# Performance work log

Hardware: AMD Instinct MI355X
Metric: run time of the kernel (lower is better)

## Reference

```python
import jax, jax.numpy as jnp
import numpy as np

NPG = 32          # nodes per graph
G = 2048          # number of graphs
V = G * NPG       # 65536 nodes
DEG = 4           # incoming edges per node
E = V * DEG       # 262144 edges
H = 200           # hidden feat size
NODE_IN = 74
EDGE_IN = 12
N_LAYERS = 5
T = 2             # readout GRU timesteps


def setup_inputs() -> dict:
    key = jax.random.key(0)
    ks = jax.random.split(key, 24)

    def p(k, shape, s=0.1):
        return jax.random.normal(k, shape, jnp.float32) * s

    node_feat = jax.random.normal(ks[0], (V, NODE_IN), jnp.float32)
    edge_feat = jax.random.normal(ks[1], (E, EDGE_IN), jnp.float32)
    # graph structure: each node gets DEG incoming edges from random nodes of the same graph
    dst = jnp.repeat(jnp.arange(V, dtype=jnp.int32), DEG)
    src = (dst // NPG) * NPG + jax.random.randint(ks[2], (E,), 0, NPG, dtype=jnp.int32)
    graph_id = jnp.arange(V, dtype=jnp.int32) // NPG

    return dict(
        node_feat=node_feat, edge_feat=edge_feat, src=src, dst=dst, graph_id=graph_id,
        node_W=p(ks[3], (NODE_IN, H)), node_b=p(ks[4], (H,)),
        edge_W=p(ks[5], (EDGE_IN, H)), edge_b=p(ks[6], (H,)),
        gnn_W=p(ks[7], (N_LAYERS, H, H)), gnn_b=p(ks[8], (N_LAYERS, H)),
        lg_W=p(ks[9], (T, 2 * H, 1)), lg_b=p(ks[10], (T, 1)),
        pr_W=p(ks[11], (T, H, H)), pr_b=p(ks[12], (T, H)),
        W_ih=p(ks[13], (T, 3 * H, H)), W_hh=p(ks[14], (T, 3 * H, H)),
        b_ih=p(ks[15], (T, 3 * H)), b_hh=p(ks[16], (T, 3 * H)),
    )


def reference(node_feat, edge_feat, src, dst, graph_id,
              node_W, node_b, edge_W, edge_b, gnn_W, gnn_b,
              lg_W, lg_b, pr_W, pr_b, W_ih, W_hh, b_ih, b_hh):
    # embedding (dropout layers are identity at eval)
    h = node_feat @ node_W + node_b        # [V, H]
    eh = edge_feat @ edge_W + edge_b       # [E, H]

    # GCN layers with edge features, aggr == 'no_relu'
    for i in range(N_LAYERS):
        m = h[src] + eh                                              # u_add_e, [E, H]
        mx = jax.ops.segment_max(m, dst, num_segments=V)             # edge_softmax over incoming edges
        ex = jnp.exp(m - mx[dst])
        den = jax.ops.segment_sum(ex, dst, num_segments=V)
        a = ex / den[dst]
        agg = jax.ops.segment_sum(m * a, dst, num_segments=V)        # [V, H]
        h = jax.nn.relu(agg @ gnn_W[i] + gnn_b[i]) + h               # mlp + relu + residual

    # AttentiveFP readout
    gf = jax.ops.segment_sum(h, graph_id, num_segments=G)            # [G, H]
    for t in range(T):
        zin = jnp.concatenate([jax.nn.relu(gf)[graph_id], h], axis=1)  # [V, 2H]
        z = jax.nn.leaky_relu(zin @ lg_W[t] + lg_b[t])                  # [V, 1]
        zmax = jax.ops.segment_max(z, graph_id, num_segments=G)        # softmax_nodes
        e = jnp.exp(z - zmax[graph_id])
        a = e / jax.ops.segment_sum(e, graph_id, num_segments=G)[graph_id]
        hv = h @ pr_W[t] + pr_b[t]
        ctx = jax.nn.elu(jax.ops.segment_sum(hv * a, graph_id, num_segments=G))  # [G, H]
        # torch GRUCell: gates ordered (r, z, n)
        gi = ctx @ W_ih[t].T + b_ih[t]
        gh = gf @ W_hh[t].T + b_hh[t]
        ir, iz, inn = jnp.split(gi, 3, axis=1)
        hr, hz, hn = jnp.split(gh, 3, axis=1)
        r = jax.nn.sigmoid(ir + hr)
        u = jax.nn.sigmoid(iz + hz)
        n = jnp.tanh(inn + r * hn)
        gf = (1.0 - u) * n + u * gf
    return gf
```

## Files before the change

kernel.cpp:

```cpp
#include <hip/hip_runtime.h>
#include <hip/hip_bf16.h>
#include <math.h>

#define V 65536
#define G 2048
#define NPG 32
#define DEG 4
#define NE (V*DEG)
#define H 200
#define NODE_IN 74
#define EDGE_IN 12
#define NL 5

#define KP 224
#define NP 208
#define AGSC 101
#define EK 32
#define HS 200

typedef __attribute__((ext_vector_type(8))) short short8;
typedef __attribute__((ext_vector_type(4))) float floatx4;
typedef __attribute__((ext_vector_type(2))) float float2v;

__device__ __forceinline__ float sigmoidf_(float x) { return 1.f / (1.f + __expf(-x)); }

__device__ __forceinline__ unsigned f2bf_bits(float f) {
    unsigned u = __float_as_uint(f);
    return (u + 0x7fffu + ((u >> 16) & 1u)) >> 16;
}
__device__ __forceinline__ float bf2f(unsigned bits) { return __uint_as_float(bits << 16); }
__device__ __forceinline__ unsigned lo_bits(float f, unsigned hb) {
    return f2bf_bits(f - bf2f(hb));
}

__global__ __launch_bounds__(256) void k_node_embed(const float* __restrict__ nf,
                                                    const float* __restrict__ W,
                                                    const float* __restrict__ b,
                                                    float* __restrict__ h) {
    __shared__ float fs[16][NODE_IN];
    const int tid = threadIdx.x;
    const int base = blockIdx.x * 16;
    for (int p = tid; p < 16 * NODE_IN; p += 256) {
        int n = p / NODE_IN, i = p - n * NODE_IN;
        fs[n][i] = nf[(base + n) * NODE_IN + i];
    }
    __syncthreads();
    const int j = tid;
    if (j < H) {
        float acc[16];
#pragma unroll
        for (int n = 0; n < 16; n++) acc[n] = 0.f;
        for (int i = 0; i < NODE_IN; i++) {
            float w = W[i * H + j];
#pragma unroll
            for (int n = 0; n < 16; n++) acc[n] = fmaf(fs[n][i], w, acc[n]);
        }
        float bj = b[j];
        for (int n = 0; n < 16; n++) h[(base + n) * H + j] = acc[n] + bj;
    }
}

#define EFB (NE / 256)
#define SEG_W (NL * NP * KP)
#define SEG_EW NP
__global__ __launch_bounds__(256) void k_prep(const float* __restrict__ ef,
                                              const float* __restrict__ gnnW,
                                              const float* __restrict__ eW,
                                              const float* __restrict__ eb,
                                              unsigned short* __restrict__ Aedge,
                                              unsigned short* __restrict__ WtHi,
                                              unsigned short* __restrict__ WtLo,
                                              unsigned short* __restrict__ eWp) {
    __shared__ float efs[256 * EDGE_IN];
    const int tid = threadIdx.x, blk = blockIdx.x;
    if (blk < EFB) {
        const float4* gs = (const float4*)(ef + (size_t)blk * 256 * EDGE_IN);
        float4* ds = (float4*)efs;
        for (int p = tid; p < 256 * EDGE_IN / 4; p += 256) ds[p] = gs[p];
        __syncthreads();
        unsigned hb[EDGE_IN], lb[EDGE_IN];
        for (int k = 0; k < EDGE_IN; k++) {
            float v = efs[tid * EDGE_IN + k];
            hb[k] = f2bf_bits(v);
            lb[k] = lo_bits(v, hb[k]);
        }
        unsigned w[16];
        for (int i = 0; i < 6; i++) w[i] = hb[2 * i] | (hb[2 * i + 1] << 16);
        for (int i = 0; i < 6; i++) w[6 + i] = lb[2 * i] | (lb[2 * i + 1] << 16);
        w[12] = 0x3F803F80u;
        w[13] = 0u; w[14] = 0u; w[15] = 0u;
        uint4* dst = (uint4*)(Aedge + ((size_t)blk * 256 + tid) * EK);
        dst[0] = make_uint4(w[0], w[1], w[2], w[3]);
        dst[1] = make_uint4(w[4], w[5], w[6], w[7]);
        dst[2] = make_uint4(w[8], w[9], w[10], w[11]);
        dst[3] = make_uint4(w[12], w[13], w[14], w[15]);
        return;
    }
    int idx = (blk - EFB) * 256 + tid;
    if (idx < SEG_W) {
        int l = idx / (NP * KP);
        int rem = idx - l * (NP * KP);
        int n = rem / KP;
        int k = rem - n * KP;
        float w = (n < H && k < H) ? gnnW[l * H * H + k * H + n] : 0.f;
        unsigned hb = f2bf_bits(w);
        WtHi[idx] = (unsigned short)hb;
        WtLo[idx] = (unsigned short)lo_bits(w, hb);
        return;
    }
    idx -= SEG_W;
    if (idx < SEG_EW) {
        int t = idx;
        unsigned short row[64];
        for (int i = 0; i < 64; i++) row[i] = 0;
        if (t < H) {
            for (int k = 0; k < EDGE_IN; k++) {
                float w = eW[k * H + t];
                unsigned hb = f2bf_bits(w);
                row[k] = (unsigned short)hb;
                row[12 + k] = (unsigned short)hb;
                row[32 + k] = (unsigned short)lo_bits(w, hb);
            }
            float e = eb[t];
            unsigned ebh = f2bf_bits(e);
            row[24] = (unsigned short)ebh;
            row[25] = (unsigned short)lo_bits(e, ebh);
        }
        for (int i = 0; i < 64; i++) eWp[t * 64 + i] = row[i];
    }
}

__global__ __launch_bounds__(256, 4) void k_mega(float* __restrict__ h,
                                                 const unsigned short* __restrict__ Aedge,
                                                 const unsigned short* __restrict__ eWp,
                                                 const int* __restrict__ src,
                                                 const unsigned short* __restrict__ WtHi,
                                                 const unsigned short* __restrict__ WtLo,
                                                 const float* __restrict__ gnn_b,
                                                 float* __restrict__ gf_out) {
    __shared__ alignas(16) float h_s[NPG * HS];
    __shared__ alignas(16) unsigned int aggc[NPG * AGSC];
    __shared__ alignas(16) unsigned int zpad[8];
    __shared__ unsigned char src_s[NPG * DEG];
    const int g = blockIdx.x, tid = threadIdx.x;
    const int nbase = g * NPG, ebase = g * NPG * DEG;

    const int wave = tid >> 6, lane = tid & 63;
    const int l15 = lane & 15, quad = lane >> 4;
    const int ntcnt = (wave == 0) ? 4 : 3;

    const int mtA = wave * 2, mtB = mtA + 1;
    short8 afA, afB;
    {
        const unsigned short* abase = Aedge + (size_t)ebase * EK;
        afA = *(const short8*)&abase[(16 * mtA + l15) * EK + quad * 8];
        afB = *(const short8*)&abase[(16 * mtB + l15) * EK + quad * 8];
    }
    if (tid < NPG * DEG) src_s[tid] = (unsigned char)(src[ebase + tid] - nbase);
    if (tid < 8) zpad[tid] = 0u;
    {
        const float4* hsrc = (const float4*)(h + (size_t)nbase * H);
        float4* hdst = (float4*)h_s;
        for (int p = tid; p < NPG * H / 4; p += 256) hdst[p] = hsrc[p];
    }
    __syncthreads();

    const int nodeA = 4 * mtA + quad, nodeB = 4 * mtB + quad;
    int gsA[4], gsB[4];
#pragma unroll
    for (int e = 0; e < 4; e++) {
        gsA[e] = (int)src_s[nodeA * 4 + e] * HS;
        gsB[e] = (int)src_s[nodeB * 4 + e] * HS;
    }
    unsigned short* rowA = (unsigned short*)(aggc + nodeA * AGSC);
    unsigned short* rowB = (unsigned short*)(aggc + nodeB * AGSC);
    const float2v L2E2 = {1.4426950408889634f, 1.4426950408889634f};

    const int ntb0[3] = {0, 6, 10};
    const int ntb1[3] = {6, 10, 13};
    const int ksb0[3] = {0, 3, 5};
    const int ksb1[3] = {3, 5, 7};

    for (int l = 0; l < NL; l++) {
        floatx4 acc2[2][4];
#pragma unroll
        for (int mt = 0; mt < 2; mt++)
#pragma unroll
            for (int i = 0; i < 4; i++) acc2[mt][i] = (floatx4){0.f, 0.f, 0.f, 0.f};

        const unsigned short* WH = WtHi + (size_t)l * NP * KP;
        const unsigned short* WL = WtLo + (size_t)l * NP * KP;

        for (int ch = 0; ch < 3; ch++) {
            const int nt0 = ntb0[ch], nt1 = ntb1[ch];
            const int ks0 = ksb0[ch], ks1 = ksb1[ch];

            for (int nt = nt0; nt < nt1; nt++) {
                const int jj = nt * 16 + l15;
                const int jloc = jj - nt0 * 16;
                const int jc = jj < H ? jj : H - 1;
                const int colo = (jloc >> 3) * 16 + (jloc & 7);
                const bool val = (jj < H);
                short8 b1 = *(const short8*)&eWp[(size_t)jj * 64 + quad * 8];
                short8 b2 = *(const short8*)&eWp[(size_t)jj * 64 + 32 + quad * 8];

                auto unit = [&](short8 af, const int* gs, unsigned short* rowp) {
                    floatx4 z = (floatx4){0.f, 0.f, 0.f, 0.f};
                    z = __builtin_amdgcn_mfma_f32_16x16x32_bf16(af, b1, z, 0, 0, 0);
                    z = __builtin_amdgcn_mfma_f32_16x16x32_bf16(af, b2, z, 0, 0, 0);
                    floatx4 mh4;
#pragma unroll
                    for (int e = 0; e < 4; e++) mh4[e] = h_s[gs[e] + jc];
                    float2v mlo = __builtin_shufflevector(z, z, 0, 1) +
                                  __builtin_shufflevector(mh4, mh4, 0, 1);
                    float2v mhi = __builtin_shufflevector(z, z, 2, 3) +
                                  __builtin_shufflevector(mh4, mh4, 2, 3);
                    float mx = fmaxf(fmaxf(mlo[0], mlo[1]), fmaxf(mhi[0], mhi[1]));
                    float nm = -mx * 1.4426950408889634f;
                    float2v nm2 = {nm, nm};
                    float2v dlo = mlo * L2E2 + nm2;
                    float2v dhi = mhi * L2E2 + nm2;
                    floatx4 ev;
                    ev[0] = __builtin_amdgcn_exp2f(dlo[0]);
                    ev[1] = __builtin_amdgcn_exp2f(dlo[1]);
                    ev[2] = __builtin_amdgcn_exp2f(dhi[0]);
                    ev[3] = __builtin_amdgcn_exp2f(dhi[1]);
                    float2v elo = __builtin_shufflevector(ev, ev, 0, 1);
                    float2v ehi = __builtin_shufflevector(ev, ev, 2, 3);
                    float2v dsum = elo + ehi;
                    float2v nsum = mlo * elo + mhi * ehi;
                    float den = dsum[0] + dsum[1];
                    float num = nsum[0] + nsum[1];
                    float a = __fdividef(num, den);
                    if (!val) a = 0.f;
                    __bf16 bh = (__bf16)a;
                    float r = a - (float)bh;
                    __bf16 bl = (__bf16)r;
                    rowp[colo] = __builtin_bit_cast(unsigned short, bh);
                    rowp[colo + 8] = __builtin_bit_cast(unsigned short, bl);
                };
                unit(afA, gsA, rowA);
                unit(afB, gsB, rowB);
            }
            __syncthreads();

            for (int ks = ks0; ks < ks1; ks++) {
                const int c = 4 * ks + quad;
                const int cl = c - 4 * ks0;
                short8 ah[2], al[2];
#pragma unroll
                for (int mt = 0; mt < 2; mt++) {
                    const unsigned int* ap = (c < 26) ? &aggc[(16 * mt + l15) * AGSC + cl * 8]
                                                      : (const unsigned int*)zpad;
                    ah[mt] = *(const short8*)ap;
                    al[mt] = *(const short8*)(ap + 4);
                }
#pragma unroll 4
                for (int i = 0; i < ntcnt; i++) {
                    int nt = wave + 4 * i;
                    size_t boff = (size_t)(16 * nt + l15) * KP + ks * 32 + quad * 8;
                    short8 vbh = *(const short8*)&WH[boff];
                    short8 vbl = *(const short8*)&WL[boff];
#pragma unroll
                    for (int mt = 0; mt < 2; mt++) {
                        acc2[mt][i] = __builtin_amdgcn_mfma_f32_16x16x32_bf16(ah[mt], vbh, acc2[mt][i], 0, 0, 0);
                        acc2[mt][i] = __builtin_amdgcn_mfma_f32_16x16x32_bf16(al[mt], vbh, acc2[mt][i], 0, 0, 0);
                        acc2[mt][i] = __builtin_amdgcn_mfma_f32_16x16x32_bf16(ah[mt], vbl, acc2[mt][i], 0, 0, 0);
                    }
                }
            }

            if (ch == 2) {
                for (int i = 0; i < ntcnt; i++) {
                    int nt = wave + 4 * i, jj = nt * 16 + l15;
                    if (jj < H) {
                        float bj = gnn_b[l * H + jj];
#pragma unroll
                        for (int mt = 0; mt < 2; mt++) {
#pragma unroll
                            for (int r = 0; r < 4; r++) {
                                float v = acc2[mt][i][r] + bj;
                                v = v > 0.f ? v : 0.f;
                                h_s[(16 * mt + quad * 4 + r) * HS + jj] += v;
                            }
                        }
                    }
                }
            }
            __syncthreads();
        }
    }

    {
        float4* dst = (float4*)(h + (size_t)nbase * H);
        const float4* srcp = (const float4*)h_s;
        for (int p = tid; p < NPG * H / 4; p += 256) dst[p] = srcp[p];
    }
    if (tid < H) {
        float s = 0.f;
        for (int n = 0; n < NPG; n++) s += h_s[n * HS + tid];
        gf_out[g * H + tid] = s;
    }
}

__global__ __launch_bounds__(256) void k_attn(const float* __restrict__ h,
                                              const float* __restrict__ gf,
                                              const float* __restrict__ lgW,
                                              const float* __restrict__ lgb,
                                              float* __restrict__ wh_out) {
    __shared__ float h_s[NPG][H];
    __shared__ float gf_s[H];
    __shared__ float z_s[NPG];
    __shared__ float a_s[NPG];
    __shared__ float den_s;
    const int g = blockIdx.x, tid = threadIdx.x;
    const int lane = tid & 63;

    for (int p = tid; p < NPG * H; p += 256) h_s[0][p] = h[g * NPG * H + p];
    if (tid < H) gf_s[tid] = gf[g * H + tid];
    __syncthreads();

    {
        const int n = tid >> 3, l = tid & 7;
        float p = 0.f;
        for (int jj = l; jj < H; jj += 8) {
            p = fmaf(h_s[n][jj], lgW[H + jj], p);
            p = fmaf(fmaxf(gf_s[jj], 0.f), lgW[jj], p);
        }
        p += __shfl_xor(p, 1);
        p += __shfl_xor(p, 2);
        p += __shfl_xor(p, 4);
        if (l == 0) {
            float z = p + lgb[0];
            z_s[n] = z > 0.f ? z : 0.01f * z;
        }
    }
    __syncthreads();

    if (tid < 64) {
        float z = (lane < NPG) ? z_s[lane] : -1e30f;
        float m = z;
        m = fmaxf(m, __shfl_xor(m, 1));
        m = fmaxf(m, __shfl_xor(m, 2));
        m = fmaxf(m, __shfl_xor(m, 4));
        m = fmaxf(m, __shfl_xor(m, 8));
        m = fmaxf(m, __shfl_xor(m, 16));
        float e = (lane < NPG) ? __expf(z - m) : 0.f;
        float d = e;
        d += __shfl_xor(d, 1);
        d += __shfl_xor(d, 2);
        d += __shfl_xor(d, 4);
        d += __shfl_xor(d, 8);
        d += __shfl_xor(d, 16);
        if (lane < NPG) a_s[lane] = e;
        if (lane == 0) den_s = d;
    }
    __syncthreads();

    if (tid < H) {
        float s = 0.f;
        for (int n = 0; n < NPG; n++) s = fmaf(a_s[n], h_s[n][tid], s);
        wh_out[g * H + tid] = s / den_s;
    }
}

#define GPB 8
#define GP 9
__global__ __launch_bounds__(512) void k_projgru(const float* __restrict__ wh,
                                                 const float* __restrict__ gf,
                                                 const float* __restrict__ prW,
                                                 const float* __restrict__ prb,
                                                 const float* __restrict__ Wih,
                                                 const float* __restrict__ Whh,
                                                 const float* __restrict__ bih,
                                                 const float* __restrict__ bhh,
                                                 float* __restrict__ gf_out) {
    __shared__ float wh_s[GPB][H];
    __shared__ float gfs[GPB][H];
    __shared__ float ctx_s[GPB][H];
    __shared__ float gi_s[3 * H][GP];
    __shared__ float gh_s[3 * H][GP];
    const int gbase = blockIdx.x * GPB, tid = threadIdx.x;

    for (int p = tid; p < GPB * H; p += 512) {
        wh_s[0][p] = wh[(size_t)gbase * H + p];
        gfs[0][p] = gf[(size_t)gbase * H + p];
    }
    __syncthreads();

    {
        const int j = tid;
        if (j < H) {
            float acc[GPB];
#pragma unroll
            for (int q = 0; q < GPB; q++) acc[q] = 0.f;
            for (int i = 0; i < H; i++) {
                float w = prW[i * H + j];
#pragma unroll
                for (int q = 0; q < GPB; q++) acc[q] = fmaf(wh_s[q][i], w, acc[q]);
            }
            float bj = prb[j];
            for (int q = 0; q < GPB; q++) {
                float s = acc[q] + bj;
                ctx_s[q][j] = s > 0.f ? s : __expf(s) - 1.f;
            }
        }
    }
    __syncthreads();

    for (int k = tid; k < 3 * H; k += 512) {
        float ai[GPB], ah[GPB];
        float bi = bih[k], bh = bhh[k];
#pragma unroll
        for (int q = 0; q < GPB; q++) { ai[q] = bi; ah[q] = bh; }
        const float4* wi4 = (const float4*)(Wih + (size_t)k * H);
        const float4* wh4 = (const float4*)(Whh + (size_t)k * H);
        for (int j4 = 0; j4 < H / 4; j4++) {
            float4 wi = wi4[j4];
            float4 wg = wh4[j4];
            int jj = j4 * 4;
#pragma unroll
            for (int q = 0; q < GPB; q++) {
                ai[q] = fmaf(ctx_s[q][jj + 0], wi.x, ai[q]);
                ai[q] = fmaf(ctx_s[q][jj + 1], wi.y, ai[q]);
                ai[q] = fmaf(ctx_s[q][jj + 2], wi.z, ai[q]);
                ai[q] = fmaf(ctx_s[q][jj + 3], wi.w, ai[q]);
                ah[q] = fmaf(gfs[q][jj + 0], wg.x, ah[q]);
                ah[q] = fmaf(gfs[q][jj + 1], wg.y, ah[q]);
                ah[q] = fmaf(gfs[q][jj + 2], wg.z, ah[q]);
                ah[q] = fmaf(gfs[q][jj + 3], wg.w, ah[q]);
            }
        }
#pragma unroll
        for (int q = 0; q < GPB; q++) { gi_s[k][q] = ai[q]; gh_s[k][q] = ah[q]; }
    }
    __syncthreads();

    for (int p = tid; p < GPB * H; p += 512) {
        int q = p / H, jj = p - q * H;
        float r = sigmoidf_(gi_s[jj][q] + gh_s[jj][q]);
        float u = sigmoidf_(gi_s[H + jj][q] + gh_s[H + jj][q]);
        float nn = tanhf(gi_s[2 * H + jj][q] + r * gh_s[2 * H + jj][q]);
        gf_out[(gbase + q) * H + jj] = (1.f - u) * nn + u * gfs[q][jj];
    }
}

extern "C" void kernel_launch(void* const* d_in, const int* in_sizes, int n_in,
                              void* d_out, int out_size, void* d_ws, size_t ws_size,
                              hipStream_t stream) {
    const float* node_feat = (const float*)d_in[0];
    const float* edge_feat = (const float*)d_in[1];
    const int* src = (const int*)d_in[2];
    const float* node_W = (const float*)d_in[5];
    const float* node_b = (const float*)d_in[6];
    const float* edge_W = (const float*)d_in[7];
    const float* edge_b = (const float*)d_in[8];
    const float* gnn_W = (const float*)d_in[9];
    const float* gnn_b = (const float*)d_in[10];
    const float* lg_W = (const float*)d_in[11];
    const float* lg_b = (const float*)d_in[12];
    const float* pr_W = (const float*)d_in[13];
    const float* pr_b = (const float*)d_in[14];
    const float* W_ih = (const float*)d_in[15];
    const float* W_hh = (const float*)d_in[16];
    const float* b_ih = (const float*)d_in[17];
    const float* b_hh = (const float*)d_in[18];
    float* out = (float*)d_out;

    char* ws = (char*)d_ws;
    size_t off = 0;
    auto alloc = [&](size_t bytes) { void* p = ws + off; off += (bytes + 4095) & ~(size_t)4095; return p; };
    float* h = (float*)alloc((size_t)V * H * 4);
    unsigned short* Aedge = (unsigned short*)alloc((size_t)NE * EK * 2);
    unsigned short* WtHi = (unsigned short*)alloc((size_t)NL * NP * KP * 2);
    unsigned short* WtLo = (unsigned short*)alloc((size_t)NL * NP * KP * 2);
    unsigned short* eWp = (unsigned short*)alloc((size_t)NP * 64 * 2);
    float* gf_ws = (float*)alloc((size_t)G * H * 4);
    float* wh_ws = (float*)alloc((size_t)G * H * 4);

    {
        int wblocks = (SEG_W + SEG_EW + 255) / 256;
        k_prep<<<EFB + wblocks, 256, 0, stream>>>(edge_feat, gnn_W, edge_W, edge_b,
                                                  Aedge, WtHi, WtLo, eWp);
    }
    k_node_embed<<<V / 16, 256, 0, stream>>>(node_feat, node_W, node_b, h);

    k_mega<<<G, 256, 0, stream>>>(h, Aedge, eWp, src, WtHi, WtLo, gnn_b, gf_ws);

    for (int t = 0; t < 2; t++) {
        k_attn<<<G, 256, 0, stream>>>(h, gf_ws, lg_W + (size_t)t * 2 * H, lg_b + t, wh_ws);
        float* gout = (t == 1) ? out : gf_ws;
        k_projgru<<<G / GPB, 512, 0, stream>>>(wh_ws, gf_ws, pr_W + (size_t)t * H * H,
                                               pr_b + (size_t)t * H,
                                               W_ih + (size_t)t * 3 * H * H,
                                               W_hh + (size_t)t * 3 * H * H,
                                               b_ih + (size_t)t * 3 * H,
                                               b_hh + (size_t)t * 3 * H, gout);
    }
}
```

Before: 709.7 us.

## Fuse attention readout and projection-GRU for both timesteps into one kernel

Merges the per-graph attention kernel and the projection+GRU kernel, across both readout timesteps, into a single kernel handling 8 graphs per 512-thread block. Each wave computes attention logits, softmax and the weighted sum for one graph, reading h directly from global memory. The updated graph features stay in shared memory between timesteps. This removes three kernel launches and the global round trips of wh and gf, but the attention phase now has only 256 blocks instead of 2048, which lowers parallelism.

```diff
diff --git a/kernel.cpp b/kernel.cpp
--- a/kernel.cpp
+++ b/kernel.cpp
@@ -303,145 +303,142 @@
     }
 }
 
-__global__ __launch_bounds__(256) void k_attn(const float* __restrict__ h,
-                                              const float* __restrict__ gf,
-                                              const float* __restrict__ lgW,
-                                              const float* __restrict__ lgb,
-                                              float* __restrict__ wh_out) {
-    __shared__ float h_s[NPG][H];
-    __shared__ float gf_s[H];
-    __shared__ float z_s[NPG];
-    __shared__ float a_s[NPG];
-    __shared__ float den_s;
-    const int g = blockIdx.x, tid = threadIdx.x;
-    const int lane = tid & 63;
-
-    for (int p = tid; p < NPG * H; p += 256) h_s[0][p] = h[g * NPG * H + p];
-    if (tid < H) gf_s[tid] = gf[g * H + tid];
+#define RGPB 8
+#define RGP 9
+__global__ __launch_bounds__(512) void k_readout(const float* __restrict__ h,
+                                                 const float* __restrict__ gf_in,
+                                                 const float* __restrict__ lg_W,
+                                                 const float* __restrict__ lg_b,
+                                                 const float* __restrict__ pr_W,
+                                                 const float* __restrict__ pr_b,
+                                                 const float* __restrict__ W_ih,
+                                                 const float* __restrict__ W_hh,
+                                                 const float* __restrict__ b_ih,
+                                                 const float* __restrict__ b_hh,
+                                                 float* __restrict__ out) {
+    __shared__ float gfs[RGPB][H];
+    __shared__ float wh_s[RGPB][H];
+    __shared__ float ctx_s[RGPB][H];
+    __shared__ float gi_s[3 * H][RGP];
+    __shared__ float gh_s[3 * H][RGP];
+    __shared__ float a_s[RGPB][NPG];
+    const int gbase = blockIdx.x * RGPB, tid = threadIdx.x;
+    const int wq = tid >> 6, lane = tid & 63;
+
+    for (int p = tid; p < RGPB * H; p += 512) gfs[0][p] = gf_in[(size_t)gbase * H + p];
     __syncthreads();
 
-    {
-        const int n = tid >> 3, l = tid & 7;
-        float p = 0.f;
-        for (int jj = l; jj < H; jj += 8) {
-            p = fmaf(h_s[n][jj], lgW[H + jj], p);
-            p = fmaf(fmaxf(gf_s[jj], 0.f), lgW[jj], p);
-        }
-        p += __shfl_xor(p, 1);
-        p += __shfl_xor(p, 2);
-        p += __shfl_xor(p, 4);
-        if (l == 0) {
-            float z = p + lgb[0];
-            z_s[n] = z > 0.f ? z : 0.01f * z;
-        }
-    }
-    __syncthreads();
-
-    if (tid < 64) {
-        float z = (lane < NPG) ? z_s[lane] : -1e30f;
-        float m = z;
-        m = fmaxf(m, __shfl_xor(m, 1));
-        m = fmaxf(m, __shfl_xor(m, 2));
-        m = fmaxf(m, __shfl_xor(m, 4));
-        m = fmaxf(m, __shfl_xor(m, 8));
-        m = fmaxf(m, __shfl_xor(m, 16));
-        float e = (lane < NPG) ? __expf(z - m) : 0.f;
-        float d = e;
-        d += __shfl_xor(d, 1);
-        d += __shfl_xor(d, 2);
-        d += __shfl_xor(d, 4);
-        d += __shfl_xor(d, 8);
-        d += __shfl_xor(d, 16);
-        if (lane < NPG) a_s[lane] = e;
-        if (lane == 0) den_s = d;
-    }
-    __syncthreads();
-
-    if (tid < H) {
-        float s = 0.f;
-        for (int n = 0; n < NPG; n++) s = fmaf(a_s[n], h_s[n][tid], s);
-        wh_out[g * H + tid] = s / den_s;
-    }
-}
-
-#define GPB 8
-#define GP 9
-__global__ __launch_bounds__(512) void k_projgru(const float* __restrict__ wh,
-                                                 const float* __restrict__ gf,
-                                                 const float* __restrict__ prW,
-                                                 const float* __restrict__ prb,
-                                                 const float* __restrict__ Wih,
-                                                 const float* __restrict__ Whh,
-                                                 const float* __restrict__ bih,
-                                                 const float* __restrict__ bhh,
-                                                 float* __restrict__ gf_out) {
-    __shared__ float wh_s[GPB][H];
-    __shared__ float gfs[GPB][H];
-    __shared__ float ctx_s[GPB][H];
-    __shared__ float gi_s[3 * H][GP];
-    __shared__ float gh_s[3 * H][GP];
-    const int gbase = blockIdx.x * GPB, tid = threadIdx.x;
-
-    for (int p = tid; p < GPB * H; p += 512) {
-        wh_s[0][p] = wh[(size_t)gbase * H + p];
-        gfs[0][p] = gf[(size_t)gbase * H + p];
-    }
-    __syncthreads();
-
-    {
-        const int j = tid;
-        if (j < H) {
-            float acc[GPB];
-#pragma unroll
-            for (int q = 0; q < GPB; q++) acc[q] = 0.f;
-            for (int i = 0; i < H; i++) {
-                float w = prW[i * H + j];
-#pragma unroll
-                for (int q = 0; q < GPB; q++) acc[q] = fmaf(wh_s[q][i], w, acc[q]);
-            }
-            float bj = prb[j];
-            for (int q = 0; q < GPB; q++) {
-                float s = acc[q] + bj;
-                ctx_s[q][j] = s > 0.f ? s : __expf(s) - 1.f;
-            }
-        }
-    }
-    __syncthreads();
-
-    for (int k = tid; k < 3 * H; k += 512) {
-        float ai[GPB], ah[GPB];
-        float bi = bih[k], bh = bhh[k];
-#pragma unroll
-        for (int q = 0; q < GPB; q++) { ai[q] = bi; ah[q] = bh; }
-        const float4* wi4 = (const float4*)(Wih + (size_t)k * H);
-        const float4* wh4 = (const float4*)(Whh + (size_t)k * H);
-        for (int j4 = 0; j4 < H / 4; j4++) {
-            float4 wi = wi4[j4];
-            float4 wg = wh4[j4];
-            int jj = j4 * 4;
-#pragma unroll
-            for (int q = 0; q < GPB; q++) {
-                ai[q] = fmaf(ctx_s[q][jj + 0], wi.x, ai[q]);
-                ai[q] = fmaf(ctx_s[q][jj + 1], wi.y, ai[q]);
-                ai[q] = fmaf(ctx_s[q][jj + 2], wi.z, ai[q]);
-                ai[q] = fmaf(ctx_s[q][jj + 3], wi.w, ai[q]);
-                ah[q] = fmaf(gfs[q][jj + 0], wg.x, ah[q]);
-                ah[q] = fmaf(gfs[q][jj + 1], wg.y, ah[q]);
-                ah[q] = fmaf(gfs[q][jj + 2], wg.z, ah[q]);
-                ah[q] = fmaf(gfs[q][jj + 3], wg.w, ah[q]);
-            }
-        }
-#pragma unroll
-        for (int q = 0; q < GPB; q++) { gi_s[k][q] = ai[q]; gh_s[k][q] = ah[q]; }
-    }
-    __syncthreads();
-
-    for (int p = tid; p < GPB * H; p += 512) {
-        int q = p / H, jj = p - q * H;
-        float r = sigmoidf_(gi_s[jj][q] + gh_s[jj][q]);
-        float u = sigmoidf_(gi_s[H + jj][q] + gh_s[H + jj][q]);
-        float nn = tanhf(gi_s[2 * H + jj][q] + r * gh_s[2 * H + jj][q]);
-        gf_out[(gbase + q) * H + jj] = (1.f - u) * nn + u * gfs[q][jj];
+    for (int t = 0; t < 2; t++) {
+        const float* lgW = lg_W + t * 2 * H;
+        const float lgb = lg_b[t];
+        const float* prW = pr_W + (size_t)t * H * H;
+        const float* prb = pr_b + (size_t)t * H;
+        const float* Wih = W_ih + (size_t)t * 3 * H * H;
+        const float* Whh = W_hh + (size_t)t * 3 * H * H;
+        const float* bih = b_ih + (size_t)t * 3 * H;
+        const float* bhh = b_hh + (size_t)t * 3 * H;
+
+        {
+            const int g = gbase + wq;
+            const int n = lane >> 1, half = lane & 1;
+            const float* hrow = h + ((size_t)g * NPG + n) * H;
+            float p = 0.f;
+            for (int j = half; j < H; j += 2) {
+                float gfj = gfs[wq][j];
+                p = fmaf(hrow[j], lgW[H + j], p);
+                p = fmaf(gfj > 0.f ? gfj : 0.f, lgW[j], p);
+            }
+            p += __shfl_xor(p, 1);
+            float z = p + lgb;
+            z = z > 0.f ? z : 0.01f * z;
+            float m = z;
+            m = fmaxf(m, __shfl_xor(m, 2));
+            m = fmaxf(m, __shfl_xor(m, 4));
+            m = fmaxf(m, __shfl_xor(m, 8));
+            m = fmaxf(m, __shfl_xor(m, 16));
+            m = fmaxf(m, __shfl_xor(m, 32));
+            float e = __expf(z - m);
+            float d = e;
+            d += __shfl_xor(d, 2);
+            d += __shfl_xor(d, 4);
+            d += __shfl_xor(d, 8);
+            d += __shfl_xor(d, 16);
+            d += __shfl_xor(d, 32);
+            if (half == 0) a_s[wq][n] = e / d;
+            float w0 = 0.f, w1 = 0.f, w2 = 0.f, w3 = 0.f;
+            for (int nn = 0; nn < NPG; nn++) {
+                float a = a_s[wq][nn];
+                const float* hr = h + ((size_t)g * NPG + nn) * H;
+                w0 = fmaf(a, hr[lane], w0);
+                w1 = fmaf(a, hr[lane + 64], w1);
+                w2 = fmaf(a, hr[lane + 128], w2);
+                if (lane < 8) w3 = fmaf(a, hr[lane + 192], w3);
+            }
+            wh_s[wq][lane] = w0;
+            wh_s[wq][lane + 64] = w1;
+            wh_s[wq][lane + 128] = w2;
+            if (lane < 8) wh_s[wq][lane + 192] = w3;
+        }
+        __syncthreads();
+
+        {
+            const int j = tid;
+            if (j < H) {
+                float acc[RGPB];
+#pragma unroll
+                for (int q = 0; q < RGPB; q++) acc[q] = 0.f;
+                for (int i = 0; i < H; i++) {
+                    float w = prW[i * H + j];
+#pragma unroll
+                    for (int q = 0; q < RGPB; q++) acc[q] = fmaf(wh_s[q][i], w, acc[q]);
+                }
+                float bj = prb[j];
+                for (int q = 0; q < RGPB; q++) {
+                    float s = acc[q] + bj;
+                    ctx_s[q][j] = s > 0.f ? s : __expf(s) - 1.f;
+                }
+            }
+        }
+        __syncthreads();
+
+        for (int k = tid; k < 3 * H; k += 512) {
+            float ai[RGPB], ah[RGPB];
+            float bi = bih[k], bh = bhh[k];
+#pragma unroll
+            for (int q = 0; q < RGPB; q++) { ai[q] = bi; ah[q] = bh; }
+            const float4* wi4 = (const float4*)(Wih + (size_t)k * H);
+            const float4* wh4 = (const float4*)(Whh + (size_t)k * H);
+            for (int j4 = 0; j4 < H / 4; j4++) {
+                float4 wi = wi4[j4];
+                float4 wg = wh4[j4];
+                int jj = j4 * 4;
+#pragma unroll
+                for (int q = 0; q < RGPB; q++) {
+                    ai[q] = fmaf(ctx_s[q][jj + 0], wi.x, ai[q]);
+                    ai[q] = fmaf(ctx_s[q][jj + 1], wi.y, ai[q]);
+                    ai[q] = fmaf(ctx_s[q][jj + 2], wi.z, ai[q]);
+                    ai[q] = fmaf(ctx_s[q][jj + 3], wi.w, ai[q]);
+                    ah[q] = fmaf(gfs[q][jj + 0], wg.x, ah[q]);
+                    ah[q] = fmaf(gfs[q][jj + 1], wg.y, ah[q]);
+                    ah[q] = fmaf(gfs[q][jj + 2], wg.z, ah[q]);
+                    ah[q] = fmaf(gfs[q][jj + 3], wg.w, ah[q]);
+                }
+            }
+#pragma unroll
+            for (int q = 0; q < RGPB; q++) { gi_s[k][q] = ai[q]; gh_s[k][q] = ah[q]; }
+        }
+        __syncthreads();
+
+        for (int p = tid; p < RGPB * H; p += 512) {
+            int q = p / H, jj = p - q * H;
+            float r = sigmoidf_(gi_s[jj][q] + gh_s[jj][q]);
+            float u = sigmoidf_(gi_s[H + jj][q] + gh_s[H + jj][q]);
+            float nn = tanhf(gi_s[2 * H + jj][q] + r * gh_s[2 * H + jj][q]);
+            float res = (1.f - u) * nn + u * gfs[q][jj];
+            gfs[q][jj] = res;
+            if (t == 1) out[(size_t)(gbase + q) * H + jj] = res;
+        }
+        __syncthreads();
     }
 }
 
@@ -476,7 +473,6 @@
     unsigned short* WtLo = (unsigned short*)alloc((size_t)NL * NP * KP * 2);
     unsigned short* eWp = (unsigned short*)alloc((size_t)NP * 64 * 2);
     float* gf_ws = (float*)alloc((size_t)G * H * 4);
-    float* wh_ws = (float*)alloc((size_t)G * H * 4);
 
     {
         int wblocks = (SEG_W + SEG_EW + 255) / 256;
@@ -487,14 +483,6 @@
 
     k_mega<<<G, 256, 0, stream>>>(h, Aedge, eWp, src, WtHi, WtLo, gnn_b, gf_ws);
 
-    for (int t = 0; t < 2; t++) {
-        k_attn<<<G, 256, 0, stream>>>(h, gf_ws, lg_W + (size_t)t * 2 * H, lg_b + t, wh_ws);
-        float* gout = (t == 1) ? out : gf_ws;
-        k_projgru<<<G / GPB, 512, 0, stream>>>(wh_ws, gf_ws, pr_W + (size_t)t * H * H,
-                                               pr_b + (size_t)t * H,
-                                               W_ih + (size_t)t * 3 * H * H,
-                                               W_hh + (size_t)t * 3 * H * H,
-                                               b_ih + (size_t)t * 3 * H,
-                                               b_hh + (size_t)t * 3 * H, gout);
-    }
-}
+    k_readout<<<G / RGPB, 512, 0, stream>>>(h, gf_ws, lg_W, lg_b, pr_W, pr_b,
+                                            W_ih, W_hh, b_ih, b_hh, out);
+}
```

New measurement: 744.2 us. +4.9%, slower.

## Fuse node embedding into prep kernel and first attention readout into GNN kernel

Applied to the files above, without the earlier changes.

Merges the node-embedding kernel into the prep kernel as extra blocks, and folds the first timestep's attention readout (logit, softmax over nodes, weighted sum) into the tail of the mega GNN kernel, which already holds h in shared memory. This removes two kernel launches and the re-read of h from global memory for the first attention pass. It reuses the aggc shared buffer for scratch and adds work to the tail of the mega kernel. The wh is computed before projection, the same quantity k_attn writes.

```diff
diff --git a/kernel.cpp b/kernel.cpp
--- a/kernel.cpp
+++ b/kernel.cpp
@@ -33,47 +33,52 @@
     return f2bf_bits(f - bf2f(hb));
 }
 
-__global__ __launch_bounds__(256) void k_node_embed(const float* __restrict__ nf,
-                                                    const float* __restrict__ W,
-                                                    const float* __restrict__ b,
-                                                    float* __restrict__ h) {
-    __shared__ float fs[16][NODE_IN];
-    const int tid = threadIdx.x;
-    const int base = blockIdx.x * 16;
-    for (int p = tid; p < 16 * NODE_IN; p += 256) {
-        int n = p / NODE_IN, i = p - n * NODE_IN;
-        fs[n][i] = nf[(base + n) * NODE_IN + i];
-    }
-    __syncthreads();
-    const int j = tid;
-    if (j < H) {
-        float acc[16];
-#pragma unroll
-        for (int n = 0; n < 16; n++) acc[n] = 0.f;
-        for (int i = 0; i < NODE_IN; i++) {
-            float w = W[i * H + j];
-#pragma unroll
-            for (int n = 0; n < 16; n++) acc[n] = fmaf(fs[n][i], w, acc[n]);
-        }
-        float bj = b[j];
-        for (int n = 0; n < 16; n++) h[(base + n) * H + j] = acc[n] + bj;
-    }
-}
-
 #define EFB (NE / 256)
 #define SEG_W (NL * NP * KP)
 #define SEG_EW NP
-__global__ __launch_bounds__(256) void k_prep(const float* __restrict__ ef,
-                                              const float* __restrict__ gnnW,
-                                              const float* __restrict__ eW,
-                                              const float* __restrict__ eb,
-                                              unsigned short* __restrict__ Aedge,
-                                              unsigned short* __restrict__ WtHi,
-                                              unsigned short* __restrict__ WtLo,
-                                              unsigned short* __restrict__ eWp) {
-    __shared__ float efs[256 * EDGE_IN];
+#define WBLOCKS ((SEG_W + SEG_EW + 255) / 256)
+#define EMBB (V / 16)
+__global__ __launch_bounds__(256) void k_prep_embed(const float* __restrict__ ef,
+                                                    const float* __restrict__ gnnW,
+                                                    const float* __restrict__ eW,
+                                                    const float* __restrict__ eb,
+                                                    const float* __restrict__ nf,
+                                                    const float* __restrict__ nW,
+                                                    const float* __restrict__ nb,
+                                                    unsigned short* __restrict__ Aedge,
+                                                    unsigned short* __restrict__ WtHi,
+                                                    unsigned short* __restrict__ WtLo,
+                                                    unsigned short* __restrict__ eWp,
+                                                    float* __restrict__ h) {
+    __shared__ float smem[256 * EDGE_IN];
     const int tid = threadIdx.x, blk = blockIdx.x;
+
+    if (blk >= EFB + WBLOCKS) {
+        float (*fs)[NODE_IN] = (float (*)[NODE_IN])smem;
+        const int base = (blk - EFB - WBLOCKS) * 16;
+        for (int p = tid; p < 16 * NODE_IN; p += 256) {
+            int n = p / NODE_IN, i = p - n * NODE_IN;
+            fs[n][i] = nf[(base + n) * NODE_IN + i];
+        }
+        __syncthreads();
+        const int j = tid;
+        if (j < H) {
+            float acc[16];
+#pragma unroll
+            for (int n = 0; n < 16; n++) acc[n] = 0.f;
+            for (int i = 0; i < NODE_IN; i++) {
+                float w = nW[i * H + j];
+#pragma unroll
+                for (int n = 0; n < 16; n++) acc[n] = fmaf(fs[n][i], w, acc[n]);
+            }
+            float bj = nb[j];
+            for (int n = 0; n < 16; n++) h[(base + n) * H + j] = acc[n] + bj;
+        }
+        return;
+    }
+
     if (blk < EFB) {
+        float* efs = smem;
         const float4* gs = (const float4*)(ef + (size_t)blk * 256 * EDGE_IN);
         float4* ds = (float4*)efs;
         for (int p = tid; p < 256 * EDGE_IN / 4; p += 256) ds[p] = gs[p];
@@ -137,7 +142,10 @@
                                                  const unsigned short* __restrict__ WtHi,
                                                  const unsigned short* __restrict__ WtLo,
                                                  const float* __restrict__ gnn_b,
-                                                 float* __restrict__ gf_out) {
+                                                 float* __restrict__ gf_out,
+                                                 const float* __restrict__ lgW,
+                                                 const float* __restrict__ lgb,
+                                                 float* __restrict__ wh_out) {
     __shared__ alignas(16) float h_s[NPG * HS];
     __shared__ alignas(16) unsigned int aggc[NPG * AGSC];
     __shared__ alignas(16) unsigned int zpad[8];
@@ -296,10 +304,56 @@
         const float4* srcp = (const float4*)h_s;
         for (int p = tid; p < NPG * H / 4; p += 256) dst[p] = srcp[p];
     }
+    float* gf_s = (float*)aggc;
+    float* z_s = gf_s + 224;
+    float* a_s = gf_s + 256;
+    float* den_p = gf_s + 288;
     if (tid < H) {
         float s = 0.f;
         for (int n = 0; n < NPG; n++) s += h_s[n * HS + tid];
         gf_out[g * H + tid] = s;
+        gf_s[tid] = s;
+    }
+    __syncthreads();
+    {
+        const int n = tid >> 3, l8 = tid & 7;
+        float p = 0.f;
+        for (int jj = l8; jj < H; jj += 8) {
+            p = fmaf(h_s[n * HS + jj], lgW[H + jj], p);
+            p = fmaf(fmaxf(gf_s[jj], 0.f), lgW[jj], p);
+        }
+        p += __shfl_xor(p, 1);
+        p += __shfl_xor(p, 2);
+        p += __shfl_xor(p, 4);
+        if (l8 == 0) {
+            float z = p + lgb[0];
+            z_s[n] = z > 0.f ? z : 0.01f * z;
+        }
+    }
+    __syncthreads();
+    if (tid < 64) {
+        float z = (lane < NPG) ? z_s[lane] : -1e30f;
+        float m = z;
+        m = fmaxf(m, __shfl_xor(m, 1));
+        m = fmaxf(m, __shfl_xor(m, 2));
+        m = fmaxf(m, __shfl_xor(m, 4));
+        m = fmaxf(m, __shfl_xor(m, 8));
+        m = fmaxf(m, __shfl_xor(m, 16));
+        float e = (lane < NPG) ? __expf(z - m) : 0.f;
+        float d = e;
+        d += __shfl_xor(d, 1);
+        d += __shfl_xor(d, 2);
+        d += __shfl_xor(d, 4);
+        d += __shfl_xor(d, 8);
+        d += __shfl_xor(d, 16);
+        if (lane < NPG) a_s[lane] = e;
+        if (lane == 0) den_p[0] = d;
+    }
+    __syncthreads();
+    if (tid < H) {
+        float s = 0.f;
+        for (int n = 0; n < NPG; n++) s = fmaf(a_s[n], h_s[n * HS + tid], s);
+        wh_out[g * H + tid] = s / den_p[0];
     }
 }
 
@@ -478,23 +532,20 @@
     float* gf_ws = (float*)alloc((size_t)G * H * 4);
     float* wh_ws = (float*)alloc((size_t)G * H * 4);
 
-    {
-        int wblocks = (SEG_W + SEG_EW + 255) / 256;
-        k_prep<<<EFB + wblocks, 256, 0, stream>>>(edge_feat, gnn_W, edge_W, edge_b,
-                                                  Aedge, WtHi, WtLo, eWp);
-    }
-    k_node_embed<<<V / 16, 256, 0, stream>>>(node_feat, node_W, node_b, h);
-
-    k_mega<<<G, 256, 0, stream>>>(h, Aedge, eWp, src, WtHi, WtLo, gnn_b, gf_ws);
-
-    for (int t = 0; t < 2; t++) {
-        k_attn<<<G, 256, 0, stream>>>(h, gf_ws, lg_W + (size_t)t * 2 * H, lg_b + t, wh_ws);
-        float* gout = (t == 1) ? out : gf_ws;
-        k_projgru<<<G / GPB, 512, 0, stream>>>(wh_ws, gf_ws, pr_W + (size_t)t * H * H,
-                                               pr_b + (size_t)t * H,
-                                               W_ih + (size_t)t * 3 * H * H,
-                                               W_hh + (size_t)t * 3 * H * H,
-                                               b_ih + (size_t)t * 3 * H,
-                                               b_hh + (size_t)t * 3 * H, gout);
-    }
-}
+    k_prep_embed<<<EFB + WBLOCKS + EMBB, 256, 0, stream>>>(
+        edge_feat, gnn_W, edge_W, edge_b, node_feat, node_W, node_b,
+        Aedge, WtHi, WtLo, eWp, h);
+
+    k_mega<<<G, 256, 0, stream>>>(h, Aedge, eWp, src, WtHi, WtLo, gnn_b, gf_ws,
+                                  lg_W, lg_b, wh_ws);
+
+    k_projgru<<<G / GPB, 512, 0, stream>>>(wh_ws, gf_ws, pr_W, pr_b,
+                                           W_ih, W_hh, b_ih, b_hh, gf_ws);
+    k_attn<<<G, 256, 0, stream>>>(h, gf_ws, lg_W + 2 * H, lg_b + 1, wh_ws);
+    k_projgru<<<G / GPB, 512, 0, stream>>>(wh_ws, gf_ws, pr_W + (size_t)H * H,
+                                           pr_b + H,
+                                           W_ih + (size_t)3 * H * H,
+                                           W_hh + (size_t)3 * H * H,
+                                           b_ih + 3 * H,
+                                           b_hh + 3 * H, out);
+}
```

Result: faster. 643.1 us (-9.4%).
